# Performance work log

Measured on AMD Instinct MI355X. Metric: run time of the kernel, lower is better.

The kernel has to match this reference:

```python
import jax, jax.numpy as jnp
import numpy as np

B, S, H, E = 32, 4096, 512, 512

def setup_inputs() -> dict:
    key = jax.random.key(0)
    ks = jax.random.split(key, 11)
    sc = 1.0 / np.sqrt(H)
    return {
        "context": jax.random.normal(ks[0], (B, S, H), jnp.float32),
        "h": jax.random.normal(ks[1], (B, H), jnp.float32),
        "x": jax.random.normal(ks[2], (B, E), jnp.float32),
        "We": jax.random.normal(ks[3], (H, H), jnp.float32) * sc,
        "be": jax.random.normal(ks[4], (H,), jnp.float32) * sc,
        "Wd": jax.random.normal(ks[5], (H, H), jnp.float32) * sc,
        "bd": jax.random.normal(ks[6], (H,), jnp.float32) * sc,
        "Wv": jax.random.normal(ks[7], (H,), jnp.float32) * sc,
        "bv": jax.random.normal(ks[8], (1,), jnp.float32) * sc,
        "Wr": jax.random.normal(ks[9], (2 * H, 2 * H + E), jnp.float32) * (1.0 / np.sqrt(2 * H + E)),
        "br": jax.random.normal(ks[10], (2 * H,), jnp.float32) * sc,
    }

def reference(context, h, x, We, be, Wd, bd, Wv, bv, Wr, br):
    # gamma_encoder: [B,S,H]; gamma_decoder: [B,1,H]
    ge = jnp.einsum('bsh,kh->bsk', context, We) + be
    gd = h @ Wd.T + bd
    # additive scores -> [B,S]
    scores = jnp.einsum('bsh,h->bs', jnp.tanh(ge + gd[:, None, :]), Wv) + bv[0]
    weights = jax.nn.softmax(scores, axis=1)
    # context vector c_t: [B,H]
    c_t = jnp.einsum('bs,bsh->bh', weights, context)
    # linear_r on [c_t, h, x] -> [B,2H]
    r_t = jnp.concatenate([c_t, h, x], axis=1) @ Wr.T + br
    # maxout over pairs: view [B,H,2].max(-1)
    output = jnp.max(r_t.reshape(-1, r_t.shape[1] // 2, 2), axis=2)
    return (output, weights)
```

## Files before the change

kernel.cpp:

```cpp
#include <hip/hip_runtime.h>

typedef __attribute__((ext_vector_type(8))) short bf16x8;
typedef __attribute__((ext_vector_type(16))) float f32x16;

typedef __attribute__((address_space(3))) unsigned int lds_u32;
typedef __attribute__((address_space(1))) unsigned int glb_u32;

union frag_u { bf16x8 v; unsigned int u[4]; };

__device__ inline unsigned int cvt_pk_bf16(float lo, float hi){
  unsigned int r;
  asm("v_cvt_pk_bf16_f32 %0, %1, %2" : "=v"(r) : "v"(lo), "v"(hi));
  return r;
}
__device__ inline bf16x8 pack8(float4 a, float4 b){
  union { unsigned int u[4]; bf16x8 v; } r;
  r.u[0]=cvt_pk_bf16(a.x,a.y); r.u[1]=cvt_pk_bf16(a.z,a.w);
  r.u[2]=cvt_pk_bf16(b.x,b.y); r.u[3]=cvt_pk_bf16(b.z,b.w);
  return r.v;
}
__device__ inline float fast_tanh(float x){
  float e = __builtin_amdgcn_exp2f(x * 2.8853900817779268f);
  return 1.0f - 2.0f * __builtin_amdgcn_rcpf(e + 1.0f);
}
#define PIN8(F) asm volatile("" : "+v"((F).u[0]), "+v"((F).u[1]), \
                                  "+v"((F).u[2]), "+v"((F).u[3]))

__global__ __launch_bounds__(256) void we_conv(const float* __restrict__ We,
                                               uint4* __restrict__ weFrag){
  int gid = blockIdx.x * 256 + threadIdx.x;
  int l  = gid & 63;
  int nc = gid >> 11;
  int t  = (gid >> 6) & 31;
  int colv = nc*32 + (l & 31);
  int k = t*16 + (l >> 5)*8;
  const float4* src = (const float4*)(We + colv*512 + k);
  float4 f0 = src[0], f1 = src[1];
  weFrag[gid] = make_uint4(cvt_pk_bf16(f0.x,f0.y), cvt_pk_bf16(f0.z,f0.w),
                           cvt_pk_bf16(f1.x,f1.y), cvt_pk_bf16(f1.z,f1.w));
}

__global__ __launch_bounds__(256) void gd_kernel(const float* __restrict__ hvec,
                                                 const float* __restrict__ Wd,
                                                 const float* __restrict__ bd,
                                                 const float* __restrict__ be,
                                                 float* __restrict__ gd){
  __shared__ float hs[512];
  int b = blockIdx.x >> 2, kc = blockIdx.x & 3;
  int tid = threadIdx.x;
  hs[tid]       = hvec[b*512 + tid];
  hs[tid + 256] = hvec[b*512 + 256 + tid];
  __syncthreads();
  int k  = kc*128 + (tid >> 1);
  int hh = (tid & 1) * 256;
  const float4* wrow = (const float4*)(Wd + (size_t)k*512 + hh);
  const float4* hv4  = (const float4*)(hs + hh);
  float acc = 0.f;
  #pragma unroll 8
  for (int i = 0; i < 64; ++i){
    float4 w = wrow[i]; float4 u = hv4[i];
    acc += w.x*u.x + w.y*u.y + w.z*u.z + w.w*u.w;
  }
  acc += __shfl_xor(acc, 1);
  if ((tid & 1) == 0) gd[b*512 + k] = acc + bd[k] + be[k];
}

__global__ __launch_bounds__(256, 2) void score_kernel(
    const float* __restrict__ ctx, const uint4* __restrict__ weFrag,
    const float* __restrict__ gd, const float* __restrict__ Wv,
    float* __restrict__ scores){
  __shared__ char lds[2*32768 + 4096];
  char* ldsB = lds;
  float* gdwv = (float*)(lds + 65536);

  const int tid  = threadIdx.x;
  const int wid  = tid >> 6;
  const int lane = tid & 63;
  const int bid  = blockIdx.x;
  const int row0 = bid * 128;
  const int b    = bid >> 5;
  const int col  = lane & 31;
  const int hi   = lane >> 5;

  #define ISSUE(NC, BUF) do { \
    const char* _g = (const char*)weFrag + (size_t)(NC)*32768 + wid*8192 + lane*16; \
    char* _l = ldsB + (BUF)*32768 + wid*8192; \
    _Pragma("unroll") \
    for (int _i = 0; _i < 8; ++_i) \
      __builtin_amdgcn_global_load_lds((const glb_u32*)(_g + _i*1024), \
                                       (lds_u32*)(_l + _i*1024), 16, 0, 0); \
  } while(0)

  ISSUE(0, 0);

  if (tid < 128) ((float4*)gdwv)[tid] = ((const float4*)(gd + b*512))[tid];
  else           ((float4*)gdwv)[tid] = ((const float4*)Wv)[tid - 128];

  frag_u afrag[32];
  {
    const float4* ap = (const float4*)(ctx + (size_t)(row0 + wid*32 + col)*512 + hi*8);
    #pragma unroll
    for (int t = 0; t < 32; ++t){
      afrag[t].v = pack8(ap[t*4], ap[t*4 + 1]);
      PIN8(afrag[t]);
    }
  }

  asm volatile("s_waitcnt lgkmcnt(0)" ::: "memory");

  float sc[16];
  #pragma unroll
  for (int r = 0; r < 16; ++r) sc[r] = 0.f;

  for (int nc = 0; nc < 16; ++nc){
    asm volatile("s_waitcnt vmcnt(0)" ::: "memory");
    __builtin_amdgcn_s_barrier();
    if (nc < 15) ISSUE(nc + 1, (nc + 1) & 1);

    const char* bb = ldsB + (nc & 1)*32768 + lane*16;
    f32x16 accLo, accHi;
    #pragma unroll
    for (int r = 0; r < 16; ++r){ accLo[r] = 0.f; accHi[r] = 0.f; }

    frag_u c0, c1, c2, c3, n0, n1, n2, n3;
    c0.v = *(const bf16x8*)(bb +  0*1024);
    c1.v = *(const bf16x8*)(bb +  8*1024);
    c2.v = *(const bf16x8*)(bb + 16*1024);
    c3.v = *(const bf16x8*)(bb + 24*1024);
    PIN8(c0); PIN8(c1); PIN8(c2); PIN8(c3);

    #pragma unroll
    for (int g = 0; g < 8; ++g){
      if (g < 7){
        n0.v = *(const bf16x8*)(bb + (g + 1     )*1024);
        n1.v = *(const bf16x8*)(bb + (g + 1 +  8)*1024);
        n2.v = *(const bf16x8*)(bb + (g + 1 + 16)*1024);
        n3.v = *(const bf16x8*)(bb + (g + 1 + 24)*1024);
      }
      __builtin_amdgcn_s_setprio(1);
      accLo = __builtin_amdgcn_mfma_f32_32x32x16_bf16(afrag[g     ].v, c0.v, accLo, 0, 0, 0);
      accHi = __builtin_amdgcn_mfma_f32_32x32x16_bf16(afrag[g + 16].v, c2.v, accHi, 0, 0, 0);
      accLo = __builtin_amdgcn_mfma_f32_32x32x16_bf16(afrag[g +  8].v, c1.v, accLo, 0, 0, 0);
      accHi = __builtin_amdgcn_mfma_f32_32x32x16_bf16(afrag[g + 24].v, c3.v, accHi, 0, 0, 0);
      __builtin_amdgcn_s_setprio(0);
      if (g < 7){
        PIN8(n0); PIN8(n1); PIN8(n2); PIN8(n3);
        c0 = n0; c1 = n1; c2 = n2; c3 = n3;
      }
    }

    float gdv = gdwv[nc*32 + col];
    float wvv = gdwv[512 + nc*32 + col];
    #pragma unroll
    for (int r = 0; r < 16; ++r)
      sc[r] += fast_tanh(accLo[r] + accHi[r] + gdv) * wvv;
  }
  #undef ISSUE

  #pragma unroll
  for (int r = 0; r < 16; ++r){
    #pragma unroll
    for (int m = 1; m <= 16; m <<= 1) sc[r] += __shfl_xor(sc[r], m);
  }
  if (col == 0){
    float* so = scores + row0 + wid*32 + 4*hi;
    #pragma unroll
    for (int r = 0; r < 16; ++r)
      so[(r & 3) + 8*(r >> 2)] = sc[r];
  }
}

__global__ __launch_bounds__(256) void softmax_kernel(const float* __restrict__ scores,
                                                      float* __restrict__ weights){
  __shared__ float red[8];
  int b = blockIdx.x, tid = threadIdx.x;
  const float4* src = (const float4*)(scores + b*4096);
  float4* dst = (float4*)(weights + b*4096);
  float4 v[4];
  float m = -1e30f;
  #pragma unroll
  for (int i = 0; i < 4; ++i){
    v[i] = src[tid + i*256];
    m = fmaxf(m, fmaxf(fmaxf(v[i].x, v[i].y), fmaxf(v[i].z, v[i].w)));
  }
  #pragma unroll
  for (int o = 1; o < 64; o <<= 1) m = fmaxf(m, __shfl_xor(m, o));
  if ((tid & 63) == 0) red[tid >> 6] = m;
  __syncthreads();
  m = fmaxf(fmaxf(red[0], red[1]), fmaxf(red[2], red[3]));
  float s = 0.f;
  #pragma unroll
  for (int i = 0; i < 4; ++i){
    v[i].x = __builtin_amdgcn_exp2f((v[i].x - m) * 1.4426950408889634f);
    v[i].y = __builtin_amdgcn_exp2f((v[i].y - m) * 1.4426950408889634f);
    v[i].z = __builtin_amdgcn_exp2f((v[i].z - m) * 1.4426950408889634f);
    v[i].w = __builtin_amdgcn_exp2f((v[i].w - m) * 1.4426950408889634f);
    s += v[i].x + v[i].y + v[i].z + v[i].w;
  }
  #pragma unroll
  for (int o = 1; o < 64; o <<= 1) s += __shfl_xor(s, o);
  if ((tid & 63) == 0) red[4 + (tid >> 6)] = s;
  __syncthreads();
  s = red[4] + red[5] + red[6] + red[7];
  float inv = 1.0f / s;
  #pragma unroll
  for (int i = 0; i < 4; ++i){
    v[i].x *= inv; v[i].y *= inv; v[i].z *= inv; v[i].w *= inv;
    dst[tid + i*256] = v[i];
  }
}

__global__ __launch_bounds__(256) void ct_partial(const float* __restrict__ ctx,
                                                  const float* __restrict__ wbuf,
                                                  float* __restrict__ part){
  int bid = blockIdx.x;
  int b = bid >> 4, ch = bid & 15;
  int tid = threadIdx.x;
  int hq = tid & 127;
  int sh = tid >> 7;
  const float* wrow = wbuf + b*4096 + ch*256;
  const float4* src = (const float4*)(ctx + ((size_t)b*4096 + (size_t)ch*256)*512) + hq;
  float4 acc = {0.f,0.f,0.f,0.f};
  #pragma unroll 8
  for (int s = sh; s < 256; s += 2){
    float w = wrow[s];
    float4 c = src[(size_t)s*128];
    acc.x += w*c.x; acc.y += w*c.y; acc.z += w*c.z; acc.w += w*c.w;
  }
  ((float4*)(part + (size_t)bid*1024 + sh*512))[hq] = acc;
}

__global__ __launch_bounds__(128) void ct_reduce(const float* __restrict__ part,
                                                 float* __restrict__ ct){
  int b = blockIdx.x, tid = threadIdx.x;
  const float4* p = (const float4*)(part + (size_t)b*16384) + tid;
  float4 acc = {0.f,0.f,0.f,0.f};
  #pragma unroll
  for (int g = 0; g < 32; ++g){
    float4 v = p[g*128];
    acc.x += v.x; acc.y += v.y; acc.z += v.z; acc.w += v.w;
  }
  ((float4*)(ct + b*512))[tid] = acc;
}

__global__ __launch_bounds__(256) void final_kernel(
    const float* __restrict__ ct, const float* __restrict__ hvec,
    const float* __restrict__ x, const float* __restrict__ Wr,
    const float* __restrict__ br, float* __restrict__ out){
  __shared__ float xs[8][1536];
  int bt = blockIdx.x >> 4;
  int it = blockIdx.x & 15;
  int tid = threadIdx.x;
  int b0 = bt * 8;
  for (int idx = tid; idx < 8*1536; idx += 256){
    int bl = idx / 1536, j = idx % 1536;
    int b = b0 + bl;
    float v = (j < 512) ? ct[b*512 + j]
            : (j < 1024) ? hvec[b*512 + (j - 512)]
            : x[b*512 + (j - 1024)];
    xs[bl][j] = v;
  }
  __syncthreads();
  int i = it*64 + (tid & 63);
  int bl0 = (tid >> 6) * 2;
  const float4* wrow = (const float4*)(Wr + (size_t)i*1536);
  const float4* x0 = (const float4*)xs[bl0];
  const float4* x1 = (const float4*)xs[bl0 + 1];
  float a0 = 0.f, a1 = 0.f;
  #pragma unroll 4
  for (int k = 0; k < 384; ++k){
    float4 w = wrow[k];
    float4 u0 = x0[k], u1 = x1[k];
    a0 += w.x*u0.x + w.y*u0.y + w.z*u0.z + w.w*u0.w;
    a1 += w.x*u1.x + w.y*u1.y + w.z*u1.z + w.w*u1.w;
  }
  float bias = br[i];
  a0 += bias; a1 += bias;
  float n0 = __shfl_xor(a0, 1);
  float n1 = __shfl_xor(a1, 1);
  if ((tid & 1) == 0){
    out[(b0 + bl0    )*512 + (i >> 1)] = fmaxf(a0, n0);
    out[(b0 + bl0 + 1)*512 + (i >> 1)] = fmaxf(a1, n1);
  }
}

extern "C" void kernel_launch(void* const* d_in, const int* in_sizes, int n_in,
                              void* d_out, int out_size, void* d_ws, size_t ws_size,
                              hipStream_t stream){
  const float* ctx  = (const float*)d_in[0];
  const float* hvec = (const float*)d_in[1];
  const float* x    = (const float*)d_in[2];
  const float* We   = (const float*)d_in[3];
  const float* be   = (const float*)d_in[4];
  const float* Wd   = (const float*)d_in[5];
  const float* bd   = (const float*)d_in[6];
  const float* Wv   = (const float*)d_in[7];
  const float* Wr   = (const float*)d_in[9];
  const float* br   = (const float*)d_in[10];

  float* out     = (float*)d_out;
  float* weights = out + 32*512;

  char* ws = (char*)d_ws;
  char* weFrag  = ws;
  float* scores = (float*)(ws + (512 << 10));
  float* part   = (float*)(ws + (1024 << 10));
  float* ct     = (float*)(ws + (3 << 20));
  float* gd     = (float*)(ws + (3 << 20) + (64 << 10));

  we_conv<<<128, 256, 0, stream>>>(We, (uint4*)weFrag);
  gd_kernel<<<128, 256, 0, stream>>>(hvec, Wd, bd, be, gd);
  score_kernel<<<1024, 256, 0, stream>>>(ctx, (const uint4*)weFrag, gd, Wv, scores);
  softmax_kernel<<<32, 256, 0, stream>>>(scores, weights);
  ct_partial<<<512, 256, 0, stream>>>(ctx, weights, part);
  ct_reduce<<<32, 128, 0, stream>>>(part, ct);
  final_kernel<<<64, 256, 0, stream>>>(ct, hvec, x, Wr, br, out);
}
```

Measured before the change: 223.1 us.

## Double rows per wave in score kernel, stream We fragments from global

```diff
diff --git a/kernel.cpp b/kernel.cpp
--- a/kernel.cpp
+++ b/kernel.cpp
@@ -2,9 +2,6 @@
 
 typedef __attribute__((ext_vector_type(8))) short bf16x8;
 typedef __attribute__((ext_vector_type(16))) float f32x16;
-
-typedef __attribute__((address_space(3))) unsigned int lds_u32;
-typedef __attribute__((address_space(1))) unsigned int glb_u32;
 
 union frag_u { bf16x8 v; unsigned int u[4]; };
 
@@ -12,12 +9,6 @@
   unsigned int r;
   asm("v_cvt_pk_bf16_f32 %0, %1, %2" : "=v"(r) : "v"(lo), "v"(hi));
   return r;
-}
-__device__ inline bf16x8 pack8(float4 a, float4 b){
-  union { unsigned int u[4]; bf16x8 v; } r;
-  r.u[0]=cvt_pk_bf16(a.x,a.y); r.u[1]=cvt_pk_bf16(a.z,a.w);
-  r.u[2]=cvt_pk_bf16(b.x,b.y); r.u[3]=cvt_pk_bf16(b.z,b.w);
-  return r.v;
 }
 __device__ inline float fast_tanh(float x){
   float e = __builtin_amdgcn_exp2f(x * 2.8853900817779268f);
@@ -65,83 +56,93 @@
   if ((tid & 1) == 0) gd[b*512 + k] = acc + bd[k] + be[k];
 }
 
-__global__ __launch_bounds__(256, 2) void score_kernel(
+__global__ __launch_bounds__(256, 1) void score_kernel(
     const float* __restrict__ ctx, const uint4* __restrict__ weFrag,
     const float* __restrict__ gd, const float* __restrict__ Wv,
     float* __restrict__ scores){
-  __shared__ char lds[2*32768 + 4096];
-  char* ldsB = lds;
-  float* gdwv = (float*)(lds + 65536);
+  __shared__ char lds[65536];
 
   const int tid  = threadIdx.x;
   const int wid  = tid >> 6;
   const int lane = tid & 63;
   const int bid  = blockIdx.x;
-  const int row0 = bid * 128;
-  const int b    = bid >> 5;
+  const int row0 = bid * 256;
+  const int b    = bid >> 4;
   const int col  = lane & 31;
   const int hi   = lane >> 5;
 
-  #define ISSUE(NC, BUF) do { \
-    const char* _g = (const char*)weFrag + (size_t)(NC)*32768 + wid*8192 + lane*16; \
-    char* _l = ldsB + (BUF)*32768 + wid*8192; \
-    _Pragma("unroll") \
-    for (int _i = 0; _i < 8; ++_i) \
-      __builtin_amdgcn_global_load_lds((const glb_u32*)(_g + _i*1024), \
-                                       (lds_u32*)(_l + _i*1024), 16, 0, 0); \
-  } while(0)
-
-  ISSUE(0, 0);
-
-  if (tid < 128) ((float4*)gdwv)[tid] = ((const float4*)(gd + b*512))[tid];
-  else           ((float4*)gdwv)[tid] = ((const float4*)Wv)[tid - 128];
-
-  frag_u afrag[32];
-  {
-    const float4* ap = (const float4*)(ctx + (size_t)(row0 + wid*32 + col)*512 + hi*8);
-    #pragma unroll
-    for (int t = 0; t < 32; ++t){
-      afrag[t].v = pack8(ap[t*4], ap[t*4 + 1]);
-      PIN8(afrag[t]);
-    }
-  }
-
-  asm volatile("s_waitcnt lgkmcnt(0)" ::: "memory");
-
-  float sc[16];
-  #pragma unroll
-  for (int r = 0; r < 16; ++r) sc[r] = 0.f;
+  frag_u af0[32], af1[32];
+
+  for (int w = 0; w < 4; ++w){
+    const float* srcBase = ctx + (size_t)(row0 + w*64) * 512;
+    #pragma unroll
+    for (int i = 0; i < 16; ++i){
+      int idx = i*256 + tid;
+      int r = idx >> 6, c8 = idx & 63;
+      const float4* s4 = (const float4*)(srcBase + r*512 + c8*8);
+      float4 f0 = s4[0], f1 = s4[1];
+      unsigned int p0 = cvt_pk_bf16(f0.x, f0.y);
+      unsigned int p1 = cvt_pk_bf16(f0.z, f0.w);
+      unsigned int p2 = cvt_pk_bf16(f1.x, f1.y);
+      unsigned int p3 = cvt_pk_bf16(f1.z, f1.w);
+      int byte = (c8*16) ^ ((r & 7) << 4);
+      *(uint4*)(lds + r*1024 + byte) = make_uint4(p0, p1, p2, p3);
+    }
+    __syncthreads();
+    if (wid == w){
+      #pragma unroll
+      for (int t = 0; t < 32; ++t){
+        int r0 = lane & 31;
+        int r1 = 32 + r0;
+        int byte = t*32 + hi*16;
+        af0[t].v = *(const bf16x8*)(lds + r0*1024 + (byte ^ ((r0 & 7) << 4)));
+        af1[t].v = *(const bf16x8*)(lds + r1*1024 + (byte ^ ((r1 & 7) << 4)));
+        PIN8(af0[t]); PIN8(af1[t]);
+      }
+    }
+    __syncthreads();
+  }
+
+  float sc0[16], sc1[16];
+  #pragma unroll
+  for (int r = 0; r < 16; ++r){ sc0[r] = 0.f; sc1[r] = 0.f; }
+
+  const char* wfBase = (const char*)weFrag + lane*16;
 
   for (int nc = 0; nc < 16; ++nc){
-    asm volatile("s_waitcnt vmcnt(0)" ::: "memory");
-    __builtin_amdgcn_s_barrier();
-    if (nc < 15) ISSUE(nc + 1, (nc + 1) & 1);
-
-    const char* bb = ldsB + (nc & 1)*32768 + lane*16;
-    f32x16 accLo, accHi;
-    #pragma unroll
-    for (int r = 0; r < 16; ++r){ accLo[r] = 0.f; accHi[r] = 0.f; }
+    const char* bp = wfBase + (size_t)nc*32768;
+
+    float gdv = gd[b*512 + nc*32 + col];
+    float wvv = Wv[nc*32 + col];
 
     frag_u c0, c1, c2, c3, n0, n1, n2, n3;
-    c0.v = *(const bf16x8*)(bb +  0*1024);
-    c1.v = *(const bf16x8*)(bb +  8*1024);
-    c2.v = *(const bf16x8*)(bb + 16*1024);
-    c3.v = *(const bf16x8*)(bb + 24*1024);
+    c0.v = *(const bf16x8*)(bp +  0*1024);
+    c1.v = *(const bf16x8*)(bp +  8*1024);
+    c2.v = *(const bf16x8*)(bp + 16*1024);
+    c3.v = *(const bf16x8*)(bp + 24*1024);
     PIN8(c0); PIN8(c1); PIN8(c2); PIN8(c3);
+
+    f32x16 aLo, aHi;
+    #pragma unroll
+    for (int r = 0; r < 16; ++r){ aLo[r] = 0.f; aHi[r] = 0.f; }
 
     #pragma unroll
     for (int g = 0; g < 8; ++g){
       if (g < 7){
-        n0.v = *(const bf16x8*)(bb + (g + 1     )*1024);
-        n1.v = *(const bf16x8*)(bb + (g + 1 +  8)*1024);
-        n2.v = *(const bf16x8*)(bb + (g + 1 + 16)*1024);
-        n3.v = *(const bf16x8*)(bb + (g + 1 + 24)*1024);
+        n0.v = *(const bf16x8*)(bp + (g + 1     )*1024);
+        n1.v = *(const bf16x8*)(bp + (g + 1 +  8)*1024);
+        n2.v = *(const bf16x8*)(bp + (g + 1 + 16)*1024);
+        n3.v = *(const bf16x8*)(bp + (g + 1 + 24)*1024);
       }
       __builtin_amdgcn_s_setprio(1);
-      accLo = __builtin_amdgcn_mfma_f32_32x32x16_bf16(afrag[g     ].v, c0.v, accLo, 0, 0, 0);
-      accHi = __builtin_amdgcn_mfma_f32_32x32x16_bf16(afrag[g + 16].v, c2.v, accHi, 0, 0, 0);
-      accLo = __builtin_amdgcn_mfma_f32_32x32x16_bf16(afrag[g +  8].v, c1.v, accLo, 0, 0, 0);
-      accHi = __builtin_amdgcn_mfma_f32_32x32x16_bf16(afrag[g + 24].v, c3.v, accHi, 0, 0, 0);
+      aLo = __builtin_amdgcn_mfma_f32_32x32x16_bf16(af0[g     ].v, c0.v, aLo, 0, 0, 0);
+      aHi = __builtin_amdgcn_mfma_f32_32x32x16_bf16(af1[g     ].v, c0.v, aHi, 0, 0, 0);
+      aLo = __builtin_amdgcn_mfma_f32_32x32x16_bf16(af0[g +  8].v, c1.v, aLo, 0, 0, 0);
+      aHi = __builtin_amdgcn_mfma_f32_32x32x16_bf16(af1[g +  8].v, c1.v, aHi, 0, 0, 0);
+      aLo = __builtin_amdgcn_mfma_f32_32x32x16_bf16(af0[g + 16].v, c2.v, aLo, 0, 0, 0);
+      aHi = __builtin_amdgcn_mfma_f32_32x32x16_bf16(af1[g + 16].v, c2.v, aHi, 0, 0, 0);
+      aLo = __builtin_amdgcn_mfma_f32_32x32x16_bf16(af0[g + 24].v, c3.v, aLo, 0, 0, 0);
+      aHi = __builtin_amdgcn_mfma_f32_32x32x16_bf16(af1[g + 24].v, c3.v, aHi, 0, 0, 0);
       __builtin_amdgcn_s_setprio(0);
       if (g < 7){
         PIN8(n0); PIN8(n1); PIN8(n2); PIN8(n3);
@@ -149,24 +150,28 @@
       }
     }
 
-    float gdv = gdwv[nc*32 + col];
-    float wvv = gdwv[512 + nc*32 + col];
-    #pragma unroll
-    for (int r = 0; r < 16; ++r)
-      sc[r] += fast_tanh(accLo[r] + accHi[r] + gdv) * wvv;
-  }
-  #undef ISSUE
+    #pragma unroll
+    for (int r = 0; r < 16; ++r){
+      sc0[r] += fast_tanh(aLo[r] + gdv) * wvv;
+      sc1[r] += fast_tanh(aHi[r] + gdv) * wvv;
+    }
+  }
 
   #pragma unroll
   for (int r = 0; r < 16; ++r){
     #pragma unroll
-    for (int m = 1; m <= 16; m <<= 1) sc[r] += __shfl_xor(sc[r], m);
+    for (int m = 1; m <= 16; m <<= 1){
+      sc0[r] += __shfl_xor(sc0[r], m);
+      sc1[r] += __shfl_xor(sc1[r], m);
+    }
   }
   if (col == 0){
-    float* so = scores + row0 + wid*32 + 4*hi;
-    #pragma unroll
-    for (int r = 0; r < 16; ++r)
-      so[(r & 3) + 8*(r >> 2)] = sc[r];
+    float* so = scores + row0 + wid*64 + 4*hi;
+    #pragma unroll
+    for (int r = 0; r < 16; ++r){
+      so[     (r & 3) + 8*(r >> 2)] = sc0[r];
+      so[32 + (r & 3) + 8*(r >> 2)] = sc1[r];
+    }
   }
 }
 
@@ -310,7 +315,7 @@
 
   we_conv<<<128, 256, 0, stream>>>(We, (uint4*)weFrag);
   gd_kernel<<<128, 256, 0, stream>>>(hvec, Wd, bd, be, gd);
-  score_kernel<<<1024, 256, 0, stream>>>(ctx, (const uint4*)weFrag, gd, Wv, scores);
+  score_kernel<<<512, 256, 0, stream>>>(ctx, (const uint4*)weFrag, gd, Wv, scores);
   softmax_kernel<<<32, 256, 0, stream>>>(scores, weights);
   ct_partial<<<512, 256, 0, stream>>>(ctx, weights, part);
   ct_reduce<<<32, 128, 0, stream>>>(part, ct);
```

Measured after the change: 388.4 us. 1.74x slower.

## Fuse context-vector accumulation into score kernel with online-softmax partials

Applied to the files above, without the earlier changes.

```diff
diff --git a/kernel.cpp b/kernel.cpp
--- a/kernel.cpp
+++ b/kernel.cpp
@@ -25,6 +25,7 @@
 }
 #define PIN8(F) asm volatile("" : "+v"((F).u[0]), "+v"((F).u[1]), \
                                   "+v"((F).u[2]), "+v"((F).u[3]))
+#define LOG2E 1.4426950408889634f
 
 __global__ __launch_bounds__(256) void we_conv(const float* __restrict__ We,
                                                uint4* __restrict__ weFrag){
@@ -68,8 +69,12 @@
 __global__ __launch_bounds__(256, 2) void score_kernel(
     const float* __restrict__ ctx, const uint4* __restrict__ weFrag,
     const float* __restrict__ gd, const float* __restrict__ Wv,
-    float* __restrict__ scores){
+    float* __restrict__ scores, float* __restrict__ ctp,
+    float* __restrict__ MS){
   __shared__ char lds[2*32768 + 4096];
+  __shared__ float sc_lds[128];
+  __shared__ float w_lds[128];
+  __shared__ float red2[2];
   char* ldsB = lds;
   float* gdwv = (float*)(lds + 65536);
 
@@ -165,82 +170,112 @@
   if (col == 0){
     float* so = scores + row0 + wid*32 + 4*hi;
     #pragma unroll
-    for (int r = 0; r < 16; ++r)
-      so[(r & 3) + 8*(r >> 2)] = sc[r];
-  }
-}
-
-__global__ __launch_bounds__(256) void softmax_kernel(const float* __restrict__ scores,
+    for (int r = 0; r < 16; ++r){
+      int rr = (r & 3) + 8*(r >> 2);
+      so[rr] = sc[r];
+      sc_lds[wid*32 + 4*hi + rr] = sc[r];
+    }
+  }
+  __syncthreads();
+
+  float M = -1e30f;
+  {
+    const float4* s4 = (const float4*)sc_lds;
+    #pragma unroll
+    for (int i = 0; i < 32; ++i){
+      float4 v = s4[i];
+      M = fmaxf(M, fmaxf(fmaxf(v.x, v.y), fmaxf(v.z, v.w)));
+    }
+  }
+  if (tid < 128){
+    float w = __builtin_amdgcn_exp2f((sc_lds[tid] - M) * LOG2E);
+    w_lds[tid] = w;
+    #pragma unroll
+    for (int o = 1; o < 64; o <<= 1) w += __shfl_xor(w, o);
+    if ((tid & 63) == 0) red2[tid >> 6] = w;
+  }
+  __syncthreads();
+  float S_blk = red2[0] + red2[1];
+
+  float ctpA = 0.f, ctpB = 0.f;
+  #pragma unroll
+  for (int p = 0; p < 2; ++p){
+    if ((wid >> 1) == p){
+      int rl = (wid & 1)*32 + col;
+      char* dst = ldsB + rl*1024;
+      int swz = (rl & 7) << 4;
+      #pragma unroll
+      for (int t = 0; t < 32; ++t)
+        *(uint4*)(dst + ((t*32 + hi*16) ^ swz)) = *(uint4*)&afrag[t].u[0];
+    }
+    __syncthreads();
+    const float* wp = w_lds + p*64;
+    #pragma unroll 8
+    for (int r = 0; r < 64; ++r){
+      unsigned int u = *(const unsigned int*)(ldsB + r*1024 + ((tid*4) ^ ((r & 7) << 4)));
+      float cw = wp[r];
+      union { unsigned int q; float f; } flo, fhi;
+      flo.q = u << 16;
+      fhi.q = u & 0xffff0000u;
+      ctpA += cw * flo.f;
+      ctpB += cw * fhi.f;
+    }
+    __syncthreads();
+  }
+  ((float2*)(ctp + (size_t)bid*512))[tid] = make_float2(ctpA, ctpB);
+  if (tid == 0){ MS[2*bid] = M; MS[2*bid + 1] = S_blk; }
+}
+
+__global__ __launch_bounds__(256) void combine_kernel(const float* __restrict__ ctp,
+                                                      const float* __restrict__ MS,
+                                                      float* __restrict__ ct,
+                                                      float* __restrict__ mbuf){
+  __shared__ float wsh[32];
+  __shared__ float msh[2];
+  int b = blockIdx.x, tid = threadIdx.x;
+  if (tid < 64){
+    int i = tid & 31;
+    float Mi = MS[(b*32 + i)*2];
+    float Si = MS[(b*32 + i)*2 + 1];
+    float M = Mi;
+    #pragma unroll
+    for (int o = 1; o < 32; o <<= 1) M = fmaxf(M, __shfl_xor(M, o));
+    float w = __builtin_amdgcn_exp2f((Mi - M) * LOG2E);
+    float d = w * Si;
+    #pragma unroll
+    for (int o = 1; o < 32; o <<= 1) d += __shfl_xor(d, o);
+    if (tid < 32) wsh[i] = w;
+    if (tid == 0){ msh[0] = M; msh[1] = 1.0f / d; }
+  }
+  __syncthreads();
+  float invd = msh[1];
+  float a0 = 0.f, a1 = 0.f;
+  #pragma unroll
+  for (int i = 0; i < 32; ++i){
+    float2 v = ((const float2*)(ctp + (size_t)(b*32 + i)*512))[tid];
+    float w = wsh[i];
+    a0 += w * v.x; a1 += w * v.y;
+  }
+  ((float2*)(ct + b*512))[tid] = make_float2(a0 * invd, a1 * invd);
+  if (tid == 0){ mbuf[2*b] = msh[0]; mbuf[2*b + 1] = invd; }
+}
+
+__global__ __launch_bounds__(256) void weights_kernel(const float* __restrict__ scores,
+                                                      const float* __restrict__ mbuf,
                                                       float* __restrict__ weights){
-  __shared__ float red[8];
   int b = blockIdx.x, tid = threadIdx.x;
+  float M = mbuf[2*b], invd = mbuf[2*b + 1];
   const float4* src = (const float4*)(scores + b*4096);
   float4* dst = (float4*)(weights + b*4096);
-  float4 v[4];
-  float m = -1e30f;
   #pragma unroll
   for (int i = 0; i < 4; ++i){
-    v[i] = src[tid + i*256];
-    m = fmaxf(m, fmaxf(fmaxf(v[i].x, v[i].y), fmaxf(v[i].z, v[i].w)));
-  }
-  #pragma unroll
-  for (int o = 1; o < 64; o <<= 1) m = fmaxf(m, __shfl_xor(m, o));
-  if ((tid & 63) == 0) red[tid >> 6] = m;
-  __syncthreads();
-  m = fmaxf(fmaxf(red[0], red[1]), fmaxf(red[2], red[3]));
-  float s = 0.f;
-  #pragma unroll
-  for (int i = 0; i < 4; ++i){
-    v[i].x = __builtin_amdgcn_exp2f((v[i].x - m) * 1.4426950408889634f);
-    v[i].y = __builtin_amdgcn_exp2f((v[i].y - m) * 1.4426950408889634f);
-    v[i].z = __builtin_amdgcn_exp2f((v[i].z - m) * 1.4426950408889634f);
-    v[i].w = __builtin_amdgcn_exp2f((v[i].w - m) * 1.4426950408889634f);
-    s += v[i].x + v[i].y + v[i].z + v[i].w;
-  }
-  #pragma unroll
-  for (int o = 1; o < 64; o <<= 1) s += __shfl_xor(s, o);
-  if ((tid & 63) == 0) red[4 + (tid >> 6)] = s;
-  __syncthreads();
-  s = red[4] + red[5] + red[6] + red[7];
-  float inv = 1.0f / s;
-  #pragma unroll
-  for (int i = 0; i < 4; ++i){
-    v[i].x *= inv; v[i].y *= inv; v[i].z *= inv; v[i].w *= inv;
-    dst[tid + i*256] = v[i];
-  }
-}
-
-__global__ __launch_bounds__(256) void ct_partial(const float* __restrict__ ctx,
-                                                  const float* __restrict__ wbuf,
-                                                  float* __restrict__ part){
-  int bid = blockIdx.x;
-  int b = bid >> 4, ch = bid & 15;
-  int tid = threadIdx.x;
-  int hq = tid & 127;
-  int sh = tid >> 7;
-  const float* wrow = wbuf + b*4096 + ch*256;
-  const float4* src = (const float4*)(ctx + ((size_t)b*4096 + (size_t)ch*256)*512) + hq;
-  float4 acc = {0.f,0.f,0.f,0.f};
-  #pragma unroll 8
-  for (int s = sh; s < 256; s += 2){
-    float w = wrow[s];
-    float4 c = src[(size_t)s*128];
-    acc.x += w*c.x; acc.y += w*c.y; acc.z += w*c.z; acc.w += w*c.w;
-  }
-  ((float4*)(part + (size_t)bid*1024 + sh*512))[hq] = acc;
-}
-
-__global__ __launch_bounds__(128) void ct_reduce(const float* __restrict__ part,
-                                                 float* __restrict__ ct){
-  int b = blockIdx.x, tid = threadIdx.x;
-  const float4* p = (const float4*)(part + (size_t)b*16384) + tid;
-  float4 acc = {0.f,0.f,0.f,0.f};
-  #pragma unroll
-  for (int g = 0; g < 32; ++g){
-    float4 v = p[g*128];
-    acc.x += v.x; acc.y += v.y; acc.z += v.z; acc.w += v.w;
-  }
-  ((float4*)(ct + b*512))[tid] = acc;
+    float4 v = src[tid + i*256];
+    v.x = __builtin_amdgcn_exp2f((v.x - M) * LOG2E) * invd;
+    v.y = __builtin_amdgcn_exp2f((v.y - M) * LOG2E) * invd;
+    v.z = __builtin_amdgcn_exp2f((v.z - M) * LOG2E) * invd;
+    v.w = __builtin_amdgcn_exp2f((v.w - M) * LOG2E) * invd;
+    dst[tid + i*256] = v;
+  }
 }
 
 __global__ __launch_bounds__(256) void final_kernel(
@@ -302,17 +337,19 @@
   float* weights = out + 32*512;
 
   char* ws = (char*)d_ws;
-  char* weFrag  = ws;
-  float* scores = (float*)(ws + (512 << 10));
-  float* part   = (float*)(ws + (1024 << 10));
-  float* ct     = (float*)(ws + (3 << 20));
-  float* gd     = (float*)(ws + (3 << 20) + (64 << 10));
+  char* weFrag   = ws;
+  float* scores  = (float*)(ws + (512 << 10));
+  float* ctp     = (float*)(ws + (1024 << 10));
+  float* MS      = (float*)(ws + (3 << 20));
+  float* mbuf    = (float*)(ws + (3 << 20) + (16 << 10));
+  float* ct      = (float*)(ws + (3 << 20) + (32 << 10));
+  float* gd      = (float*)(ws + (3 << 20) + (96 << 10));
 
   we_conv<<<128, 256, 0, stream>>>(We, (uint4*)weFrag);
   gd_kernel<<<128, 256, 0, stream>>>(hvec, Wd, bd, be, gd);
-  score_kernel<<<1024, 256, 0, stream>>>(ctx, (const uint4*)weFrag, gd, Wv, scores);
-  softmax_kernel<<<32, 256, 0, stream>>>(scores, weights);
-  ct_partial<<<512, 256, 0, stream>>>(ctx, weights, part);
-  ct_reduce<<<32, 128, 0, stream>>>(part, ct);
+  score_kernel<<<1024, 256, 0, stream>>>(ctx, (const uint4*)weFrag, gd, Wv,
+                                         scores, ctp, MS);
+  combine_kernel<<<32, 256, 0, stream>>>(ctp, MS, ct, mbuf);
+  weights_kernel<<<32, 256, 0, stream>>>(scores, mbuf, weights);
   final_kernel<<<64, 256, 0, stream>>>(ct, hvec, x, Wr, br, out);
 }
```

Result: faster. 201.1 us (-9.9%).
